# Kernel optimization log

Hardware: AMD Instinct MI355X
Metric: run time of the kernel (lower is better)

Reference implementation:

```python
import jax, jax.numpy as jnp
import numpy as np

B, N, D, OUT = 4, 4096, 2048, 2048
E, RANK, TOP_K = 8, 16, 2
ALPHA = 16.0
SCALING = ALPHA / RANK


def setup_inputs() -> dict:
    key = jax.random.key(0)
    k1, k2, k3, k4 = jax.random.split(key, 4)
    x = jax.random.normal(k1, (B, N, D), dtype=jnp.float32)
    weight = jax.random.normal(k2, (OUT, D), dtype=jnp.float32) * (1.0 / np.sqrt(D))
    router_w = jax.random.normal(k3, (E, D), dtype=jnp.float32) * 0.02
    experts_A = jax.random.normal(k4, (E, D, RANK), dtype=jnp.float32) * (1.0 / np.sqrt(RANK))
    # experts_B is zero-initialized in the module; use small random values so the
    # LoRA branch contributes non-trivially to the output for kernel testing.
    experts_B = jax.random.normal(jax.random.fold_in(key, 5), (E, RANK, OUT), dtype=jnp.float32) * 0.02
    return {"x": x, "weight": weight, "router_w": router_w,
            "experts_A": experts_A, "experts_B": experts_B}


def reference(x, weight, router_w, experts_A, experts_B):
    # base = F.linear(x, weight)  (no bias)
    base = jnp.einsum('bnd,od->bno', x, weight)
    # router logits: x @ W_r^T -> (B, N, E)
    logits = jnp.einsum('bnd,ed->bne', x, router_w)
    # top-k sparse routing: keep top-k logits, set rest to -inf, softmax
    topk_vals, topk_idx = jax.lax.top_k(logits, TOP_K)  # (B,N,K)
    keep = jax.nn.one_hot(topk_idx, E, dtype=jnp.bool_).any(axis=-2)  # (B,N,E)
    masked = jnp.where(keep, logits, -jnp.inf)
    router_weights = jax.nn.softmax(masked, axis=-1)  # (B,N,E)
    # per-expert low-rank down/up projection, weighted by router
    lora_down = jnp.einsum('bnd,edr->bner', x, experts_A)  # (B,N,E,rank)
    weighted = lora_down * router_weights[..., None]
    moe_out = jnp.einsum('bner,erd->bnd', weighted, experts_B)  # (B,N,OUT)
    return base + SCALING * moe_out
```

## Files before the change

kernel.cpp:

```cpp
#include <hip/hip_runtime.h>
#include <stdint.h>

#define D_DIM 2048
#define OUT_DIM 2048
#define NTOK 16384
#define SCALING 1.0f
#define NT32 68

typedef unsigned short u16;
typedef __attribute__((ext_vector_type(8))) short s16x8;
typedef __attribute__((ext_vector_type(4))) float f32x4;

#define WZ_OFF  0u
#define AZ_OFF  8388608u
#define BZ_OFF  8912896u
#define CZ_OFF  9437184u
#define XB_OFF  14155776u
#define WS_BIG   81264640u

__device__ inline u16 f2bf(float f) {
  union { float f; uint32_t u; } v; v.f = f;
  uint32_t u = v.u;
  u += 0x7FFFu + ((u >> 16) & 1u);
  return (u16)(u >> 16);
}

__device__ inline int swz32(int c, int row) {
  return (c & ~31) | (((((c >> 3) & 3) ^ ((row >> 1) & 3))) << 3) | (c & 7);
}

#define GLDS(gp, lp) __builtin_amdgcn_global_load_lds( \
    (const __attribute__((address_space(1))) void*)(gp), \
    (__attribute__((address_space(3))) void*)(lp), 16, 0, 0)

__global__ __launch_bounds__(256) void k_prep_a(const float* __restrict__ A,
                                                u16* __restrict__ Az) {
  int idx = blockIdx.x * 256 + threadIdx.x;
  float v = A[idx];
  int r = idx & 15;
  int d = (idx >> 4) & 2047;
  int e = idx >> 15;
  int er = e * 16 + r;
  Az[(size_t)er * D_DIM + swz32(d, er)] = f2bf(v);
}

__global__ __launch_bounds__(256) void k_router_lora(
    const float* __restrict__ x, const float* __restrict__ rw,
    const float* __restrict__ W, const float* __restrict__ Bf,
    const u16* __restrict__ Az, u16* __restrict__ xb, u16* __restrict__ Cz,
    u16* __restrict__ Wz, u16* __restrict__ Bz) {
  int bid = blockIdx.x;
  if (bid >= 256) {
    if (bid < 4352) {
      int idx = (bid - 256) * 256 + threadIdx.x;
      int o  = idx >> 9;
      int k0 = (idx & 511) * 4;
      const float4 v = *(const float4*)&W[(size_t)o * D_DIM + k0];
      int dst = swz32(k0, o);
      uint32_t p0 = (uint32_t)f2bf(v.x) | ((uint32_t)f2bf(v.y) << 16);
      uint32_t p1 = (uint32_t)f2bf(v.z) | ((uint32_t)f2bf(v.w) << 16);
      *(uint2*)&Wz[(size_t)o * D_DIM + dst] = make_uint2(p0, p1);
    } else {
      int idx = (bid - 4352) * 256 + threadIdx.x;
      float v = Bf[idx];
      int er = idx >> 11;
      int o  = idx & 2047;
      Bz[(size_t)o * 128 + swz32(er, o)] = f2bf(v);
    }
    return;
  }
  __shared__ u16 Axl[2][64 * 64];
  __shared__ u16 Bzl[2][128 * 64];
  __shared__ float w8s[64 * 8];
  int tid = threadIdx.x, lane = tid & 63, wid = tid >> 6;
  int t0 = bid * 64;
  const int l15 = lane & 15;
  const int c4 = (tid & 15) * 4;
  const int rbase = tid >> 4;

  f32x4 acc[8];
#pragma unroll
  for (int n = 0; n < 8; ++n) acc[n] = (f32x4){0.f, 0.f, 0.f, 0.f};
  float lgp[4][8];
#pragma unroll
  for (int i = 0; i < 4; ++i)
#pragma unroll
    for (int e = 0; e < 8; ++e) lgp[i][e] = 0.f;

  float4 xn[4];
  auto ldx = [&](int kc) {
    if (kc > 31) kc = 31;
#pragma unroll
    for (int i = 0; i < 4; ++i)
      xn[i] = *(const float4*)&x[(size_t)(t0 + i * 16 + rbase) * D_DIM + kc * 64 + c4];
  };
  auto use = [&](int kc, int buf) {
    bool real = (kc <= 31);
    if (!real) kc = 31;
    if (real) {
#pragma unroll
      for (int e = 0; e < 8; ++e) {
        float4 rv = *(const float4*)&rw[(size_t)e * D_DIM + kc * 64 + c4];
#pragma unroll
        for (int i = 0; i < 4; ++i) {
          lgp[i][e] = fmaf(xn[i].x, rv.x, lgp[i][e]);
          lgp[i][e] = fmaf(xn[i].y, rv.y, lgp[i][e]);
          lgp[i][e] = fmaf(xn[i].z, rv.z, lgp[i][e]);
          lgp[i][e] = fmaf(xn[i].w, rv.w, lgp[i][e]);
        }
      }
    }
#pragma unroll
    for (int i = 0; i < 4; ++i) {
      int row = i * 16 + rbase;
      uint32_t p0 = (uint32_t)f2bf(xn[i].x) | ((uint32_t)f2bf(xn[i].y) << 16);
      uint32_t p1 = (uint32_t)f2bf(xn[i].z) | ((uint32_t)f2bf(xn[i].w) << 16);
      *(uint2*)&xb[(size_t)(t0 + row) * D_DIM + swz32(kc * 64 + c4, row)] =
          make_uint2(p0, p1);
      *(uint2*)&Axl[buf][row * 64 + swz32(c4, row)] = make_uint2(p0, p1);
    }
#pragma unroll
    for (int i = 0; i < 4; ++i) {
      const u16* g = Az + (size_t)(i * 32 + (tid >> 3)) * D_DIM + kc * 64 + (tid & 7) * 8;
      GLDS(g, &Bzl[buf][0] + i * 2048 + tid * 8);
    }
  };

  ldx(0);
  use(0, 0);
  asm volatile("s_waitcnt vmcnt(0) lgkmcnt(0)" ::: "memory");
  __builtin_amdgcn_s_barrier();

  const int g = (lane >> 4) ^ ((l15 >> 1) & 3);
  for (int kc = 0; kc < 32; ++kc) {
    int cur = kc & 1;
    ldx(kc + 1);
#pragma unroll
    for (int kk = 0; kk < 2; ++kk) {
      s16x8 af = *(const s16x8*)&Axl[cur][(wid * 16 + l15) * 64 + kk * 32 + g * 8];
#pragma unroll
      for (int nf = 0; nf < 8; ++nf) {
        s16x8 bf = *(const s16x8*)&Bzl[cur][(nf * 16 + l15) * 64 + kk * 32 + g * 8];
        acc[nf] = __builtin_amdgcn_mfma_f32_16x16x32_bf16(af, bf, acc[nf], 0, 0, 0);
      }
    }
    use(kc + 1, cur ^ 1);
    asm volatile("s_waitcnt vmcnt(0) lgkmcnt(0)" ::: "memory");
    __builtin_amdgcn_s_barrier();
  }

#pragma unroll
  for (int i = 0; i < 4; ++i) {
#pragma unroll
    for (int e = 0; e < 8; ++e) {
      float v = lgp[i][e];
      v += __shfl_xor(v, 1, 64);
      v += __shfl_xor(v, 2, 64);
      v += __shfl_xor(v, 4, 64);
      v += __shfl_xor(v, 8, 64);
      lgp[i][e] = v;
    }
    float l0 = lgp[i][0]; int i0 = 0;
#pragma unroll
    for (int e = 1; e < 8; ++e) if (lgp[i][e] > l0) { l0 = lgp[i][e]; i0 = e; }
    float l1 = -3e38f; int i1 = 0;
#pragma unroll
    for (int e = 0; e < 8; ++e) if (e != i0 && lgp[i][e] > l1) { l1 = lgp[i][e]; i1 = e; }
    float e1 = expf(l1 - l0);
    float inv = 1.f / (1.f + e1);
    if (l15 < 8) {
      int row = i * 16 + rbase;
      w8s[row * 8 + l15] =
          (l15 == i0) ? inv * SCALING : (l15 == i1) ? e1 * inv * SCALING : 0.f;
    }
  }
  __syncthreads();

#pragma unroll
  for (int q = 0; q < 4; ++q) {
    int rl = wid * 16 + (lane >> 4) * 4 + q;
#pragma unroll
    for (int nf = 0; nf < 8; ++nf) {
      float v = acc[nf][q] * w8s[rl * 8 + nf];
      int er = nf * 16 + l15;
      Cz[(size_t)(t0 + rl) * 128 + swz32(er, rl)] = f2bf(v);
    }
  }
}

__global__ __launch_bounds__(512, 2) void k_main32(const u16* __restrict__ xb,
                                                   const u16* __restrict__ Wz,
                                                   const u16* __restrict__ Cz,
                                                   const u16* __restrict__ Bz,
                                                   float* __restrict__ out) {
  __shared__ u16 AL[4][8192];
  __shared__ u16 BL[4][8192];
  const int tid = threadIdx.x, lane = tid & 63;
  const int wid = tid >> 6, wm = wid >> 2, wn = wid & 3;
  int bid = blockIdx.x;
  int swz = (bid & 7) * 64 + (bid >> 3);
  int mt = swz >> 3, nt = swz & 7;
  int t0 = mt * 256, o0 = nt * 256;
  const int l15 = lane & 15;
  const int gA = (lane >> 4) ^ ((l15 >> 1) & 3);
  const int aoff = (wm * 128 + l15) * 32 + gA * 8;
  const int boff = (wn * 64 + l15) * 32 + gA * 8;
  const int srow = tid >> 2, sc8 = (tid & 3) * 8;

  f32x4 acc[8][4];
#pragma unroll
  for (int m = 0; m < 8; ++m)
#pragma unroll
    for (int n = 0; n < 4; ++n) acc[m][n] = (f32x4){0.f, 0.f, 0.f, 0.f};
  s16x8 aA[8], bA[4], aB[8], bB[4];

  auto stg = [&](int t, int bufi) {
    if (t > NT32 - 1) t = NT32 - 1;
    const u16 *sa, *sb; int lda, ldb, ca;
    if (t < 64) { sa = xb; lda = D_DIM; sb = Wz; ldb = D_DIM; ca = t * 32; }
    else        { sa = Cz; lda = 128;   sb = Bz; ldb = 128;   ca = (t - 64) * 32; }
#pragma unroll
    for (int i = 0; i < 2; ++i) {
      const u16* g = sa + (size_t)(t0 + i * 128 + srow) * lda + ca + sc8;
      GLDS(g, &AL[bufi][0] + i * 4096 + tid * 8);
    }
#pragma unroll
    for (int i = 0; i < 2; ++i) {
      const u16* g = sb + (size_t)(o0 + i * 128 + srow) * ldb + ca + sc8;
      GLDS(g, &BL[bufi][0] + i * 4096 + tid * 8);
    }
  };

#define RD(av, bv, bufi) do {                                           \
    const u16* ap_ = &AL[bufi][aoff];                                   \
    const u16* bp_ = &BL[bufi][boff];                                   \
    _Pragma("unroll") for (int i_ = 0; i_ < 8; ++i_)                    \
      av[i_] = *(const s16x8*)(ap_ + i_ * 512);                         \
    _Pragma("unroll") for (int j_ = 0; j_ < 4; ++j_)                    \
      bv[j_] = *(const s16x8*)(bp_ + j_ * 512);                         \
  } while (0)

#define MM(av, bv) do {                                                 \
    _Pragma("unroll") for (int mf_ = 0; mf_ < 8; ++mf_)                 \
      _Pragma("unroll") for (int nf_ = 0; nf_ < 4; ++nf_)               \
        acc[mf_][nf_] = __builtin_amdgcn_mfma_f32_16x16x32_bf16(        \
            av[mf_], bv[nf_], acc[mf_][nf_], 0, 0, 0);                  \
  } while (0)

  stg(0, 0); stg(1, 1); stg(2, 2);
  asm volatile("s_waitcnt vmcnt(4)" ::: "memory");
  __builtin_amdgcn_s_barrier();
  RD(aA, bA, 0);

  for (int jj = 0; jj < NT32; jj += 2) {
    RD(aB, bB, (jj + 1) & 3);
    MM(aA, bA);
    stg(jj + 3, (jj + 3) & 3);
    asm volatile("s_waitcnt vmcnt(4)" ::: "memory");
    __builtin_amdgcn_s_barrier();
    RD(aA, bA, (jj + 2) & 3);
    MM(aB, bB);
    stg(jj + 4, (jj + 4) & 3);
    asm volatile("s_waitcnt vmcnt(4)" ::: "memory");
    __builtin_amdgcn_s_barrier();
  }
  asm volatile("s_waitcnt vmcnt(0) lgkmcnt(0)" ::: "memory");
#undef RD
#undef MM

#pragma unroll
  for (int mf = 0; mf < 8; ++mf)
#pragma unroll
    for (int q = 0; q < 4; ++q) {
      int row = t0 + wm * 128 + mf * 16 + (lane >> 4) * 4 + q;
#pragma unroll
      for (int nf = 0; nf < 4; ++nf) {
        int col = o0 + wn * 64 + nf * 16 + l15;
        out[(size_t)row * OUT_DIM + col] = acc[mf][nf][q];
      }
    }
}

extern "C" void kernel_launch(void* const* d_in, const int* in_sizes, int n_in,
                              void* d_out, int out_size, void* d_ws, size_t ws_size,
                              hipStream_t stream) {
  const float* x  = (const float*)d_in[0];
  const float* W  = (const float*)d_in[1];
  const float* rw = (const float*)d_in[2];
  const float* eA = (const float*)d_in[3];
  const float* eB = (const float*)d_in[4];
  float* out = (float*)d_out;
  char* ws = (char*)d_ws;
  if (ws_size < WS_BIG) return;

  u16* Wz = (u16*)(ws + WZ_OFF);
  u16* Az = (u16*)(ws + AZ_OFF);
  u16* Bz = (u16*)(ws + BZ_OFF);
  u16* Cz = (u16*)(ws + CZ_OFF);
  u16* xb = (u16*)(ws + XB_OFF);

  k_prep_a<<<1024, 256, 0, stream>>>(eA, Az);
  k_router_lora<<<5376, 256, 0, stream>>>(x, rw, W, eB, Az, xb, Cz, Wz, Bz);
  k_main32<<<512, 512, 0, stream>>>(xb, Wz, Cz, Bz, out);
}
```

Before: 223.9 us.

## Load B operand directly from global into registers, drop B LDS staging

The B tile (weights and LoRA up-projection) is no longer staged through shared memory. Each wave now loads its MFMA B fragments straight from global memory into registers two k-steps ahead, and the vmcnt waits are adjusted to match. This halves LDS usage and LDS read traffic, which could raise occupancy. The cost is that the four waves sharing a B tile now load it redundantly, using less-coalesced 16-byte row loads, and register pressure goes up.

After: 251.4 us. 12.3% more time.

```diff
diff --git a/kernel.cpp b/kernel.cpp
--- a/kernel.cpp
+++ b/kernel.cpp
@@ -194,7 +194,6 @@
                                                    const u16* __restrict__ Bz,
                                                    float* __restrict__ out) {
   __shared__ u16 AL[4][8192];
-  __shared__ u16 BL[4][8192];
   const int tid = threadIdx.x, lane = tid & 63;
   const int wid = tid >> 6, wm = wid >> 2, wn = wid & 3;
   int bid = blockIdx.x;
@@ -204,40 +203,42 @@
   const int l15 = lane & 15;
   const int gA = (lane >> 4) ^ ((l15 >> 1) & 3);
   const int aoff = (wm * 128 + l15) * 32 + gA * 8;
-  const int boff = (wn * 64 + l15) * 32 + gA * 8;
   const int srow = tid >> 2, sc8 = (tid & 3) * 8;
+  const int brow = o0 + wn * 64 + l15;
 
   f32x4 acc[8][4];
 #pragma unroll
   for (int m = 0; m < 8; ++m)
 #pragma unroll
     for (int n = 0; n < 4; ++n) acc[m][n] = (f32x4){0.f, 0.f, 0.f, 0.f};
-  s16x8 aA[8], bA[4], aB[8], bB[4];
+  s16x8 aA[8], aB[8], bB0[4], bB1[4];
 
   auto stg = [&](int t, int bufi) {
     if (t > NT32 - 1) t = NT32 - 1;
-    const u16 *sa, *sb; int lda, ldb, ca;
-    if (t < 64) { sa = xb; lda = D_DIM; sb = Wz; ldb = D_DIM; ca = t * 32; }
-    else        { sa = Cz; lda = 128;   sb = Bz; ldb = 128;   ca = (t - 64) * 32; }
+    const u16* sa; int lda, ca;
+    if (t < 64) { sa = xb; lda = D_DIM; ca = t * 32; }
+    else        { sa = Cz; lda = 128;   ca = (t - 64) * 32; }
 #pragma unroll
     for (int i = 0; i < 2; ++i) {
       const u16* g = sa + (size_t)(t0 + i * 128 + srow) * lda + ca + sc8;
       GLDS(g, &AL[bufi][0] + i * 4096 + tid * 8);
     }
-#pragma unroll
-    for (int i = 0; i < 2; ++i) {
-      const u16* g = sb + (size_t)(o0 + i * 128 + srow) * ldb + ca + sc8;
-      GLDS(g, &BL[bufi][0] + i * 4096 + tid * 8);
-    }
   };
 
-#define RD(av, bv, bufi) do {                                           \
+  auto ldB = [&](int t, s16x8* bv) {
+    if (t > NT32 - 1) t = NT32 - 1;
+    const u16* sb; int ldb, ca;
+    if (t < 64) { sb = Wz; ldb = D_DIM; ca = t * 32; }
+    else        { sb = Bz; ldb = 128;   ca = (t - 64) * 32; }
+#pragma unroll
+    for (int nf = 0; nf < 4; ++nf)
+      bv[nf] = *(const s16x8*)&sb[(size_t)(brow + nf * 16) * ldb + ca + gA * 8];
+  };
+
+#define RD(av, bufi) do {                                               \
     const u16* ap_ = &AL[bufi][aoff];                                   \
-    const u16* bp_ = &BL[bufi][boff];                                   \
     _Pragma("unroll") for (int i_ = 0; i_ < 8; ++i_)                    \
       av[i_] = *(const s16x8*)(ap_ + i_ * 512);                         \
-    _Pragma("unroll") for (int j_ = 0; j_ < 4; ++j_)                    \
-      bv[j_] = *(const s16x8*)(bp_ + j_ * 512);                         \
   } while (0)
 
 #define MM(av, bv) do {                                                 \
@@ -248,20 +249,23 @@
   } while (0)
 
   stg(0, 0); stg(1, 1); stg(2, 2);
-  asm volatile("s_waitcnt vmcnt(4)" ::: "memory");
+  ldB(0, bB0); ldB(1, bB1);
+  asm volatile("s_waitcnt vmcnt(12)" ::: "memory");
   __builtin_amdgcn_s_barrier();
-  RD(aA, bA, 0);
+  RD(aA, 0);
 
   for (int jj = 0; jj < NT32; jj += 2) {
-    RD(aB, bB, (jj + 1) & 3);
-    MM(aA, bA);
+    RD(aB, (jj + 1) & 3);
+    MM(aA, bB0);
+    ldB(jj + 2, bB0);
     stg(jj + 3, (jj + 3) & 3);
-    asm volatile("s_waitcnt vmcnt(4)" ::: "memory");
+    asm volatile("s_waitcnt vmcnt(6)" ::: "memory");
     __builtin_amdgcn_s_barrier();
-    RD(aA, bA, (jj + 2) & 3);
-    MM(aB, bB);
+    RD(aA, (jj + 2) & 3);
+    MM(aB, bB1);
+    ldB(jj + 3, bB1);
     stg(jj + 4, (jj + 4) & 3);
-    asm volatile("s_waitcnt vmcnt(4)" ::: "memory");
+    asm volatile("s_waitcnt vmcnt(6)" ::: "memory");
     __builtin_amdgcn_s_barrier();
   }
   asm volatile("s_waitcnt vmcnt(0) lgkmcnt(0)" ::: "memory");
```
